# Kernel optimization log

Hardware: AMD Instinct MI355X
Metric: run time of the kernel (lower is better)

## Reference

```python
import jax, jax.numpy as jnp
import numpy as np
from jax import lax

WS = 4
HEADS = 8
DIM = 256
EPS = 1e-5


def _rel_index(ws):
    coords = np.stack(np.meshgrid(np.arange(ws), np.arange(ws), indexing='ij')).reshape(2, -1)
    rc = (coords[:, :, None] - coords[:, None, :]).transpose(1, 2, 0).astype(np.int64)
    rc[..., 0] += ws - 1
    rc[..., 1] += ws - 1
    rc[..., 0] *= 2 * ws - 1
    return jnp.asarray(rc.sum(-1))  # (ws*ws, ws*ws)

REL_IDX = _rel_index(WS)


def _bn(x, g, b, m, v):
    # inference BatchNorm2d, eps=1e-5
    s = g / jnp.sqrt(v + EPS)
    return x * s[None, :, None, None] + (b - m * s)[None, :, None, None]


def setup_inputs() -> dict:
    key = jax.random.key(0)
    ks = jax.random.split(key, 8)
    C = DIM
    return {
        'x': jax.random.normal(ks[0], (4, C, 256, 256), jnp.float32),
        'qkv_w': jax.random.normal(ks[1], (3 * C, C), jnp.float32) * 0.05,
        'qkv_b': jax.random.normal(ks[2], (3 * C,), jnp.float32) * 0.02,
        'rel_bias_table': jax.random.normal(ks[3], ((2 * WS - 1) ** 2, HEADS), jnp.float32) * 0.02,
        'gaze_pw': jax.random.normal(ks[4], (C, C), jnp.float32) * 0.05,
        'gaze_dw': jax.random.normal(ks[5], (C, 1, 3, 3), jnp.float32) * 0.05,
        'gaze_bn_g': jnp.ones((C,), jnp.float32),
        'gaze_bn_b': jnp.zeros((C,), jnp.float32),
        'gaze_bn_m': jnp.zeros((C,), jnp.float32),
        'gaze_bn_v': jnp.ones((C,), jnp.float32),
        'proj_w': jax.random.normal(ks[6], (C, C), jnp.float32) * 0.05,
        'proj_bn_g': jnp.ones((C,), jnp.float32),
        'proj_bn_b': jnp.zeros((C,), jnp.float32),
        'proj_bn_m': jnp.zeros((C,), jnp.float32),
        'proj_bn_v': jnp.ones((C,), jnp.float32),
    }


def reference(x, qkv_w, qkv_b, rel_bias_table, gaze_pw, gaze_dw, gaze_bn_g, gaze_bn_b, gaze_bn_m, gaze_bn_v, proj_w, proj_bn_g, proj_bn_b, proj_bn_m, proj_bn_v):
    B, C, H, W = x.shape
    ws, h = WS, HEADS
    d = C // h
    hh, ww = H // ws, W // ws  # H,W divisible by ws -> reflect pad in original is a no-op
    scale = d ** -0.5

    # qkv 1x1 conv
    qkv = jnp.einsum('bchw,oc->bohw', x, qkv_w) + qkv_b[None, :, None, None]
    # 'b (qkv h d) (hh ws1) (ww ws2) -> qkv (b hh ww) h (ws1 ws2) d'
    qkv = qkv.reshape(B, 3, h, d, hh, ws, ww, ws)
    qkv = qkv.transpose(1, 0, 4, 6, 2, 5, 7, 3).reshape(3, B * hh * ww, h, ws * ws, d)
    q, k, v = qkv[0], qkv[1], qkv[2]

    dots = jnp.einsum('nhqd,nhkd->nhqk', q, k) * scale
    bias = rel_bias_table[REL_IDX.reshape(-1)].reshape(ws * ws, ws * ws, h).transpose(2, 0, 1)
    attn = jax.nn.softmax(dots + bias[None], axis=-1)
    o = jnp.einsum('nhqk,nhkd->nhqd', attn, v)

    def win2img(t):  # '(b hh ww) h (ws1 ws2) d -> b (h d) (hh ws1) (ww ws2)'
        return t.reshape(B, hh, ww, h, ws, ws, d).transpose(0, 3, 6, 1, 4, 2, 5).reshape(B, C, H, W)

    attn_img = win2img(o)
    v_img = win2img(v)

    # gaze = SeparableConvBN: 1x1 pointwise -> 3x3 depthwise -> BN
    vg = jnp.einsum('bchw,oc->bohw', v_img, gaze_pw)
    vg = lax.conv_general_dilated(vg, gaze_dw, (1, 1), ((1, 1), (1, 1)),
                                  feature_group_count=C,
                                  dimension_numbers=('NCHW', 'OIHW', 'NCHW'))
    v_gaze = v_img + _bn(vg, gaze_bn_g, gaze_bn_b, gaze_bn_m, gaze_bn_v)

    # attn_x: reflect-pad bottom 1, AvgPool2d((ws,1), stride 1, pad (ws//2-1,0)), count_include_pad
    ax = jnp.pad(attn_img, ((0, 0), (0, 0), (0, 1), (0, 0)), mode='reflect')
    ax = lax.reduce_window(ax, 0.0, lax.add, (1, 1, ws, 1), (1, 1, 1, 1),
                           ((0, 0), (0, 0), (ws // 2 - 1, ws // 2 - 1), (0, 0))) / ws
    ay = jnp.pad(attn_img, ((0, 0), (0, 0), (0, 0), (0, 1)), mode='reflect')
    ay = lax.reduce_window(ay, 0.0, lax.add, (1, 1, 1, ws), (1, 1, 1, 1),
                           ((0, 0), (0, 0), (0, 0), (ws // 2 - 1, ws // 2 - 1))) / ws

    out = ax + ay + v_gaze
    out = jnp.pad(out, ((0, 0), (0, 0), (0, 1), (0, 1)), mode='reflect')  # pad_out
    out = jnp.einsum('bchw,oc->bohw', out, proj_w)  # proj 1x1 conv (no bias)
    out = _bn(out, proj_bn_g, proj_bn_b, proj_bn_m, proj_bn_v)
    # proj_drop is identity in eval mode
    return out[:, :, :H, :W]
```

## Files before the change

kernel.cpp:

```cpp
#include <hip/hip_runtime.h>


typedef float  f32x4  __attribute__((ext_vector_type(4)));
typedef __bf16 bf16x8 __attribute__((ext_vector_type(8)));
typedef __bf16 bf16x4 __attribute__((ext_vector_type(4)));

#define HW 65536
#define EPSF 1e-5f

__global__ __launch_bounds__(256) void k_prep(
    const float* __restrict__ qkv_w, const float* __restrict__ qkv_b,
    const float* __restrict__ rel_tab,
    const float* __restrict__ gaze_pw, const float* __restrict__ gaze_dw,
    const float* __restrict__ g_g, const float* __restrict__ g_b,
    const float* __restrict__ g_m, const float* __restrict__ g_v,
    const float* __restrict__ proj_w,
    const float* __restrict__ p_g, const float* __restrict__ p_b,
    const float* __restrict__ p_m, const float* __restrict__ p_v,
    __bf16* Wqkv, __bf16* Wpw, __bf16* Wproj,
    float* bqkv, float* biasT, float* dwf, float* bias_g, float* bias_p)
{
  int i = blockIdx.x * 256 + threadIdx.x;
  if (i < 196608) { Wqkv[i] = (__bf16)qkv_w[i]; return; }
  i -= 196608;
  if (i < 65536) { Wpw[i] = (__bf16)gaze_pw[i]; return; }
  i -= 65536;
  if (i < 65536) {
    int o = i >> 8;
    float s = p_g[o] * rsqrtf(p_v[o] + EPSF);
    Wproj[i] = (__bf16)(proj_w[i] * s);
    return;
  }
  i -= 65536;
  if (i < 768) { bqkv[i] = qkv_b[i]; return; }
  i -= 768;
  if (i < 2048) {
    int h = i >> 8, q = (i >> 4) & 15, k = i & 15;
    int rel = ((q >> 2) - (k >> 2) + 3) * 7 + ((q & 3) - (k & 3) + 3);
    biasT[i] = rel_tab[rel * 8 + h];
    return;
  }
  i -= 2048;
  if (i < 2304) {
    int c = i / 9;
    float s = g_g[c] * rsqrtf(g_v[c] + EPSF);
    dwf[i] = gaze_dw[i] * s;
    return;
  }
  i -= 2304;
  if (i < 256) {
    float s = g_g[i] * rsqrtf(g_v[i] + EPSF);
    bias_g[i] = g_b[i] - g_m[i] * s;
    return;
  }
  i -= 256;
  if (i < 256) {
    float s = p_g[i] * rsqrtf(p_v[i] + EPSF);
    bias_p[i] = p_b[i] - p_m[i] * s;
    return;
  }
}

#define K2_SMEM 145408

__global__ __launch_bounds__(512, 2) void k_qkv_attn(
    const float* __restrict__ x, const __bf16* __restrict__ Wqkv,
    const float* __restrict__ bqkv, const float* __restrict__ biasT,
    __bf16* __restrict__ attn_img, __bf16* __restrict__ v_img)
{
  extern __shared__ char smem[];
  __bf16* Xs  = (__bf16*)smem;
  __bf16* QKs = Xs + 64 * 264;
  __bf16* Vs  = QKs + 64 * 520;
  __bf16* Ps  = Vs + 256 * 72;
  __bf16* Os  = QKs;

  const int tid  = threadIdx.x;
  const int lane = tid & 63, wid = tid >> 6;
  const int mrow = lane & 15, kgrp = lane >> 4;
  const int b = blockIdx.z, h0 = blockIdx.y * 4, w0 = blockIdx.x * 16;

  {
    bf16x4 z4;
    z4[0] = z4[1] = z4[2] = z4[3] = (__bf16)0.f;
    *(bf16x4*)(Vs + (tid >> 1) * 72 + 64 + (tid & 1) * 4) = z4;
    bf16x8 z8;
#pragma unroll
    for (int j = 0; j < 8; ++j) z8[j] = (__bf16)0.f;
    *(bf16x8*)(Ps + tid * 8) = z8;
  }

  const float* xb = x + (size_t)b * 256 * HW + (size_t)h0 * 256 + w0;
#pragma unroll
  for (int it = 0; it < 8; ++it) {
    int idx = tid + it * 512;
    int c = idx >> 4, r = (idx >> 2) & 3, g = idx & 3;
    f32x4 v = *(const f32x4*)(xb + (size_t)c * HW + r * 256 + g * 4);
    int p = r * 16 + g * 4;
    Xs[(p + 0) * 264 + c] = (__bf16)v[0];
    Xs[(p + 1) * 264 + c] = (__bf16)v[1];
    Xs[(p + 2) * 264 + c] = (__bf16)v[2];
    Xs[(p + 3) * 264 + c] = (__bf16)v[3];
  }
  __syncthreads();

  for (int co = 0; co < 6; ++co) {
    f32x4 acc[4] = {{0.f,0.f,0.f,0.f},{0.f,0.f,0.f,0.f},
                    {0.f,0.f,0.f,0.f},{0.f,0.f,0.f,0.f}};
    const int ob = co * 128 + wid * 16;
    const __bf16* wp = Wqkv + (size_t)(ob + mrow) * 256 + kgrp * 8;
#pragma unroll
    for (int ks = 0; ks < 8; ++ks) {
      bf16x8 af = *(const bf16x8*)(wp + ks * 32);
#pragma unroll
      for (int j = 0; j < 4; ++j) {
        bf16x8 bm = *(const bf16x8*)(Xs + (j * 16 + mrow) * 264 + ks * 32 + kgrp * 8);
        acc[j] = __builtin_amdgcn_mfma_f32_16x16x32_bf16(af, bm, acc[j], 0, 0, 0);
      }
    }
    f32x4 bi = *(const f32x4*)(bqkv + ob + kgrp * 4);
    if (co < 4) {
      float sc = (co < 2) ? 0.17677669529663687f : 1.0f;
#pragma unroll
      for (int j = 0; j < 4; ++j) {
        int p = j * 16 + mrow;
        bf16x4 pk;
#pragma unroll
        for (int t = 0; t < 4; ++t) pk[t] = (__bf16)((acc[j][t] + bi[t]) * sc);
        *(bf16x4*)(QKs + p * 520 + ob + kgrp * 4) = pk;
      }
    } else {
      int cb = ob - 512 + kgrp * 4;
#pragma unroll
      for (int j = 0; j < 4; ++j) {
        int p = j * 16 + mrow;
#pragma unroll
        for (int t = 0; t < 4; ++t)
          Vs[(cb + t) * 72 + p] = (__bf16)(acc[j][t] + bi[t]);
      }
    }
  }
  __syncthreads();

  bf16x4 osav[4][2];
#pragma unroll
  for (int u = 0; u < 4; ++u) {
    int wh = wid * 4 + u;
    int win = wh >> 3, head = wh & 7;
    int ptok = (mrow >> 2) * 16 + win * 4 + (mrow & 3);
    bf16x8 kf = *(const bf16x8*)(QKs + ptok * 520 + 256 + head * 32 + kgrp * 8);
    bf16x8 qf = *(const bf16x8*)(QKs + ptok * 520 + head * 32 + kgrp * 8);
    f32x4 z4 = {0.f, 0.f, 0.f, 0.f};
    f32x4 d = __builtin_amdgcn_mfma_f32_16x16x32_bf16(kf, qf, z4, 0, 0, 0);
    f32x4 bt = *(const f32x4*)(biasT + head * 256 + mrow * 16 + kgrp * 4);
    float s0 = d[0] + bt[0], s1 = d[1] + bt[1], s2 = d[2] + bt[2], s3 = d[3] + bt[3];
    float mx = fmaxf(fmaxf(s0, s1), fmaxf(s2, s3));
    mx = fmaxf(mx, __shfl_xor(mx, 16));
    mx = fmaxf(mx, __shfl_xor(mx, 32));
    float e0 = __expf(s0 - mx), e1 = __expf(s1 - mx);
    float e2 = __expf(s2 - mx), e3 = __expf(s3 - mx);
    float sm = e0 + e1 + e2 + e3;
    sm += __shfl_xor(sm, 16);
    sm += __shfl_xor(sm, 32);
    float inv = 1.0f / sm;
    bf16x4 pk;
    pk[0] = (__bf16)(e0 * inv); pk[1] = (__bf16)(e1 * inv);
    pk[2] = (__bf16)(e2 * inv); pk[3] = (__bf16)(e3 * inv);
    *(bf16x4*)(Ps + wid * 512 + mrow * 32 + kgrp * 4) = pk;
    bf16x8 pf = *(const bf16x8*)(Ps + wid * 512 + mrow * 32 + kgrp * 8);
#pragma unroll
    for (int dt = 0; dt < 2; ++dt) {
      int c = head * 32 + dt * 16 + mrow;
      bf16x4 va = *(const bf16x4*)(Vs + c * 72 + kgrp * 32 + win * 4);
      bf16x4 vb = *(const bf16x4*)(Vs + c * 72 + kgrp * 32 + 16 + win * 4);
      bf16x8 vf;
#pragma unroll
      for (int t = 0; t < 4; ++t) { vf[t] = va[t]; vf[4 + t] = vb[t]; }
      f32x4 o = __builtin_amdgcn_mfma_f32_16x16x32_bf16(pf, vf, z4, 0, 0, 0);
      bf16x4 ok;
#pragma unroll
      for (int t = 0; t < 4; ++t) ok[t] = (__bf16)o[t];
      osav[u][dt] = ok;
    }
  }
  __syncthreads();
#pragma unroll
  for (int u = 0; u < 4; ++u) {
    int wh = wid * 4 + u, win = wh >> 3, head = wh & 7;
#pragma unroll
    for (int dt = 0; dt < 2; ++dt) {
      int c = head * 32 + dt * 16 + mrow;
      *(bf16x4*)(Os + c * 72 + kgrp * 16 + win * 4) = osav[u][dt];
    }
  }
  __syncthreads();

#pragma unroll
  for (int it = 0; it < 4; ++it) {
    int idx = tid + it * 512;
    int c = idx >> 3, seg = idx & 7;
    bf16x8 o8 = *(const bf16x8*)(Os + c * 72 + seg * 8);
    bf16x8 v8 = *(const bf16x8*)(Vs + c * 72 + seg * 8);
    size_t g = ((size_t)(b * 256 + c) * 256 + h0 + (seg >> 1)) * 256 + w0 + (seg & 1) * 8;
    *(bf16x8*)(attn_img + g) = o8;
    *(bf16x8*)(v_img + g) = v8;
  }
}

__global__ __launch_bounds__(256, 4) void k_pw(
    const __bf16* __restrict__ vimg, const __bf16* __restrict__ Wpw,
    __bf16* __restrict__ vg)
{
  __shared__ __bf16 Xs[64 * 264];
  const int tid = threadIdx.x, lane = tid & 63, wid = tid >> 6;
  const int mrow = lane & 15, kgrp = lane >> 4;
  const int b = blockIdx.z, h = blockIdx.y, w0 = blockIdx.x * 64;
  const size_t rowbase = ((size_t)(b * 256) * 256 + h) * 256 + w0;
#pragma unroll
  for (int it = 0; it < 8; ++it) {
    int idx = tid + it * 256;
    int c = idx >> 3, g = idx & 7;
    bf16x8 v = *(const bf16x8*)(vimg + rowbase + (size_t)c * HW + g * 8);
#pragma unroll
    for (int j = 0; j < 8; ++j) Xs[(g * 8 + j) * 264 + c] = v[j];
  }
  __syncthreads();
  for (int oh = 0; oh < 2; ++oh) {
    int o0 = oh * 128 + wid * 32;
    f32x4 acc[2][4];
#pragma unroll
    for (int mt = 0; mt < 2; ++mt)
#pragma unroll
      for (int nt = 0; nt < 4; ++nt) acc[mt][nt] = (f32x4){0.f, 0.f, 0.f, 0.f};
#pragma unroll
    for (int ks = 0; ks < 8; ++ks) {
      bf16x8 af[2], bm[4];
#pragma unroll
      for (int mt = 0; mt < 2; ++mt)
        af[mt] = *(const bf16x8*)(Wpw + (size_t)(o0 + mt * 16 + mrow) * 256 + ks * 32 + kgrp * 8);
#pragma unroll
      for (int nt = 0; nt < 4; ++nt)
        bm[nt] = *(const bf16x8*)(Xs + (nt * 16 + mrow) * 264 + ks * 32 + kgrp * 8);
#pragma unroll
      for (int mt = 0; mt < 2; ++mt)
#pragma unroll
        for (int nt = 0; nt < 4; ++nt)
          acc[mt][nt] = __builtin_amdgcn_mfma_f32_16x16x32_bf16(af[mt], bm[nt], acc[mt][nt], 0, 0, 0);
    }
#pragma unroll
    for (int mt = 0; mt < 2; ++mt)
#pragma unroll
      for (int nt = 0; nt < 4; ++nt)
#pragma unroll
        for (int t = 0; t < 4; ++t) {
          int o = o0 + mt * 16 + kgrp * 4 + t;
          int p = nt * 16 + mrow;
          vg[rowbase + (size_t)o * HW + p] = (__bf16)acc[mt][nt][t];
        }
  }
}

__global__ __launch_bounds__(256, 4) void k_mix(
    const __bf16* __restrict__ vg, const __bf16* __restrict__ attn,
    const __bf16* __restrict__ vimg, const float* __restrict__ dwf,
    const float* __restrict__ bias_g, __bf16* __restrict__ tout)
{
  __shared__ __bf16 VgS[18 * 256];
  __shared__ __bf16 AtS[19 * 256];
  __shared__ __bf16 ViS[16 * 256];
  const int tid = threadIdx.x;
  const int b = blockIdx.z, c = blockIdx.y, h0 = blockIdx.x * 16;
  const size_t plane = (size_t)(b * 256 + c) * HW;

  for (int idx = tid; idx < 576; idx += 256) {
    int row = idx >> 5, g = idx & 31;
    int hg = h0 - 1 + row;
    bf16x8 v;
#pragma unroll
    for (int j = 0; j < 8; ++j) v[j] = (__bf16)0.f;
    if (hg >= 0 && hg < 256)
      v = *(const bf16x8*)(vg + plane + (size_t)hg * 256 + g * 8);
    *(bf16x8*)(VgS + row * 256 + g * 8) = v;
  }
  for (int idx = tid; idx < 608; idx += 256) {
    int row = idx >> 5, g = idx & 31;
    int hg = h0 - 1 + row;
    bf16x8 v;
#pragma unroll
    for (int j = 0; j < 8; ++j) v[j] = (__bf16)0.f;
    if (hg >= 0 && hg <= 256) {
      int hs = (hg == 256) ? 254 : hg;
      v = *(const bf16x8*)(attn + plane + (size_t)hs * 256 + g * 8);
    }
    *(bf16x8*)(AtS + row * 256 + g * 8) = v;
  }
  for (int idx = tid; idx < 512; idx += 256) {
    int row = idx >> 5, g = idx & 31;
    *(bf16x8*)(ViS + row * 256 + g * 8) =
        *(const bf16x8*)(vimg + plane + (size_t)(h0 + row) * 256 + g * 8);
  }
  float kw[9];
#pragma unroll
  for (int i = 0; i < 9; ++i) kw[i] = dwf[c * 9 + i];
  const float bg = bias_g[c];
  __syncthreads();

  const int hl = tid >> 4, wb = (tid & 15) * 16;
  const __bf16* v0 = VgS + hl * 256;
  const __bf16* v1 = v0 + 256;
  const __bf16* v2 = v1 + 256;
  const __bf16* a0 = AtS + hl * 256;
  const __bf16* a1 = a0 + 256;
  const __bf16* a2 = a1 + 256;
  const __bf16* a3 = a2 + 256;
  const __bf16* vi = ViS + hl * 256;
  const size_t orow = plane + (size_t)(h0 + hl) * 256;
  for (int w8 = 0; w8 < 2; ++w8) {
    bf16x8 res;
#pragma unroll
    for (int j = 0; j < 8; ++j) {
      int w = wb + w8 * 8 + j;
      int xm = w - 1, xp = w + 1;
      float conv = kw[1] * (float)v0[w] + kw[4] * (float)v1[w] + kw[7] * (float)v2[w];
      if (xm >= 0)
        conv += kw[0] * (float)v0[xm] + kw[3] * (float)v1[xm] + kw[6] * (float)v2[xm];
      if (xp < 256)
        conv += kw[2] * (float)v0[xp] + kw[5] * (float)v1[xp] + kw[8] * (float)v2[xp];
      float ax = 0.25f * ((float)a0[w] + (float)a1[w] + (float)a2[w] + (float)a3[w]);
      float aym = (w >= 1) ? (float)a1[w - 1] : 0.f;
      float ay1 = (w + 1 <= 255) ? (float)a1[w + 1] : (float)a1[254];
      float ay2;
      int x2 = w + 2;
      if (x2 <= 255) ay2 = (float)a1[x2];
      else if (x2 == 256) ay2 = (float)a1[254];
      else ay2 = 0.f;
      float ay = 0.25f * (aym + (float)a1[w] + ay1 + ay2);
      res[j] = (__bf16)((float)vi[w] + conv + bg + ax + ay);
    }
    *(bf16x8*)(tout + orow + wb + w8 * 8) = res;
  }
}

__global__ __launch_bounds__(256, 4) void k_proj(
    const __bf16* __restrict__ tin, const __bf16* __restrict__ Wp,
    const float* __restrict__ bias_p, float* __restrict__ out)
{
  __shared__ __bf16 Xs[64 * 264];
  const int tid = threadIdx.x, lane = tid & 63, wid = tid >> 6;
  const int mrow = lane & 15, kgrp = lane >> 4;
  const int b = blockIdx.z, h = blockIdx.y, w0 = blockIdx.x * 64;
  const size_t rowbase = ((size_t)(b * 256) * 256 + h) * 256 + w0;
#pragma unroll
  for (int it = 0; it < 8; ++it) {
    int idx = tid + it * 256;
    int c = idx >> 3, g = idx & 7;
    bf16x8 v = *(const bf16x8*)(tin + rowbase + (size_t)c * HW + g * 8);
#pragma unroll
    for (int j = 0; j < 8; ++j) Xs[(g * 8 + j) * 264 + c] = v[j];
  }
  __syncthreads();
  for (int oh = 0; oh < 2; ++oh) {
    int o0 = oh * 128 + wid * 32;
    f32x4 acc[2][4];
#pragma unroll
    for (int mt = 0; mt < 2; ++mt)
#pragma unroll
      for (int nt = 0; nt < 4; ++nt) acc[mt][nt] = (f32x4){0.f, 0.f, 0.f, 0.f};
#pragma unroll
    for (int ks = 0; ks < 8; ++ks) {
      bf16x8 af[2], bm[4];
#pragma unroll
      for (int mt = 0; mt < 2; ++mt)
        af[mt] = *(const bf16x8*)(Wp + (size_t)(o0 + mt * 16 + mrow) * 256 + ks * 32 + kgrp * 8);
#pragma unroll
      for (int nt = 0; nt < 4; ++nt)
        bm[nt] = *(const bf16x8*)(Xs + (nt * 16 + mrow) * 264 + ks * 32 + kgrp * 8);
#pragma unroll
      for (int mt = 0; mt < 2; ++mt)
#pragma unroll
        for (int nt = 0; nt < 4; ++nt)
          acc[mt][nt] = __builtin_amdgcn_mfma_f32_16x16x32_bf16(af[mt], bm[nt], acc[mt][nt], 0, 0, 0);
    }
#pragma unroll
    for (int mt = 0; mt < 2; ++mt) {
      f32x4 bi = *(const f32x4*)(bias_p + o0 + mt * 16 + kgrp * 4);
#pragma unroll
      for (int nt = 0; nt < 4; ++nt)
#pragma unroll
        for (int t = 0; t < 4; ++t) {
          int o = o0 + mt * 16 + kgrp * 4 + t;
          int p = nt * 16 + mrow;
          out[rowbase + (size_t)o * HW + p] = acc[mt][nt][t] + bi[t];
        }
    }
  }
}

extern "C" void kernel_launch(void* const* d_in, const int* in_sizes, int n_in,
                              void* d_out, int out_size, void* d_ws, size_t ws_size,
                              hipStream_t stream) {
  const float* x      = (const float*)d_in[0];
  const float* qkv_w  = (const float*)d_in[1];
  const float* qkv_b  = (const float*)d_in[2];
  const float* rel    = (const float*)d_in[3];
  const float* gpw    = (const float*)d_in[4];
  const float* gdw    = (const float*)d_in[5];
  const float* gg     = (const float*)d_in[6];
  const float* gb     = (const float*)d_in[7];
  const float* gm     = (const float*)d_in[8];
  const float* gv     = (const float*)d_in[9];
  const float* pw     = (const float*)d_in[10];
  const float* pg     = (const float*)d_in[11];
  const float* pb     = (const float*)d_in[12];
  const float* pm     = (const float*)d_in[13];
  const float* pv     = (const float*)d_in[14];

  char* ws = (char*)d_ws;
  __bf16* Wqkv   = (__bf16*)(ws + 0);
  __bf16* Wpw    = (__bf16*)(ws + 393216);
  __bf16* Wproj  = (__bf16*)(ws + 524288);
  float*  bqkv   = (float*)(ws + 655360);
  float*  biasT  = (float*)(ws + 658432);
  float*  dwf    = (float*)(ws + 666624);
  float*  bias_g = (float*)(ws + 675840);
  float*  bias_p = (float*)(ws + 676864);
  __bf16* attn_img = (__bf16*)(ws + (1 << 20));
  __bf16* v_img    = attn_img + 67108864;
  __bf16* vg       = v_img + 67108864;
  __bf16* tbuf     = vg + 67108864;
  float* out = (float*)d_out;

  (void)hipFuncSetAttribute((const void*)k_qkv_attn,
                            hipFuncAttributeMaxDynamicSharedMemorySize, K2_SMEM);

  k_prep<<<1302, 256, 0, stream>>>(qkv_w, qkv_b, rel, gpw, gdw, gg, gb, gm, gv,
                                   pw, pg, pb, pm, pv,
                                   Wqkv, Wpw, Wproj, bqkv, biasT, dwf, bias_g, bias_p);

  dim3 g2(16, 64, 4);
  k_qkv_attn<<<g2, 512, K2_SMEM, stream>>>(x, Wqkv, bqkv, biasT, attn_img, v_img);

  dim3 g3(4, 256, 4);
  k_pw<<<g3, 256, 0, stream>>>(v_img, Wpw, vg);

  dim3 g4(16, 256, 4);
  k_mix<<<g4, 256, 0, stream>>>(vg, attn_img, v_img, dwf, bias_g, tbuf);

  k_proj<<<g3, 256, 0, stream>>>(tbuf, Wproj, bias_p, out);
}
```

Measured before the change: 1.754 ms.

## Stage pointwise and proj GEMM inputs through LDS transpose with vectorized stores

The pw and proj kernels now load input channels in two 128-channel chunks into a natural-layout LDS buffer, then transpose it into a pixel-major buffer using 16-byte writes, replacing scattered 2-byte LDS stores. The MFMA operands are swapped so each lane's accumulator holds consecutive pixels, which lets the epilogue write bf16x4 or f32x4 vectors instead of scalar strided stores. The qkv kernel's x load is also changed to scalar per-column loads. This costs extra syncs and an additional LDS pass, and the scalar x loads in the qkv kernel may reduce global load width.

```diff
diff --git a/kernel.cpp b/kernel.cpp
--- a/kernel.cpp
+++ b/kernel.cpp
@@ -93,14 +93,12 @@
   const float* xb = x + (size_t)b * 256 * HW + (size_t)h0 * 256 + w0;
 #pragma unroll
   for (int it = 0; it < 8; ++it) {
-    int idx = tid + it * 512;
-    int c = idx >> 4, r = (idx >> 2) & 3, g = idx & 3;
-    f32x4 v = *(const f32x4*)(xb + (size_t)c * HW + r * 256 + g * 4);
-    int p = r * 16 + g * 4;
-    Xs[(p + 0) * 264 + c] = (__bf16)v[0];
-    Xs[(p + 1) * 264 + c] = (__bf16)v[1];
-    Xs[(p + 2) * 264 + c] = (__bf16)v[2];
-    Xs[(p + 3) * 264 + c] = (__bf16)v[3];
+    int idx = it * 512 + tid;
+    int c = idx >> 4, col = idx & 15;
+    const float* px = xb + (size_t)c * HW + col;
+#pragma unroll
+    for (int r = 0; r < 4; ++r)
+      Xs[(r * 16 + col) * 264 + c] = (__bf16)px[(size_t)r * 256];
   }
   __syncthreads();
 
@@ -211,52 +209,75 @@
     const __bf16* __restrict__ vimg, const __bf16* __restrict__ Wpw,
     __bf16* __restrict__ vg)
 {
-  __shared__ __bf16 Xs[64 * 264];
+  __shared__ __bf16 Ns[128 * 72];
+  __shared__ __bf16 Xs[64 * 136];
   const int tid = threadIdx.x, lane = tid & 63, wid = tid >> 6;
   const int mrow = lane & 15, kgrp = lane >> 4;
   const int b = blockIdx.z, h = blockIdx.y, w0 = blockIdx.x * 64;
   const size_t rowbase = ((size_t)(b * 256) * 256 + h) * 256 + w0;
-#pragma unroll
-  for (int it = 0; it < 8; ++it) {
-    int idx = tid + it * 256;
-    int c = idx >> 3, g = idx & 7;
-    bf16x8 v = *(const bf16x8*)(vimg + rowbase + (size_t)c * HW + g * 8);
-#pragma unroll
-    for (int j = 0; j < 8; ++j) Xs[(g * 8 + j) * 264 + c] = v[j];
-  }
-  __syncthreads();
+
+  f32x4 acc[2][2][4];
+#pragma unroll
+  for (int oh = 0; oh < 2; ++oh)
+#pragma unroll
+    for (int mt = 0; mt < 2; ++mt)
+#pragma unroll
+      for (int nt = 0; nt < 4; ++nt) acc[oh][mt][nt] = (f32x4){0.f, 0.f, 0.f, 0.f};
+
+  for (int kc = 0; kc < 2; ++kc) {
+#pragma unroll
+    for (int it = 0; it < 4; ++it) {
+      int idx = it * 256 + tid;
+      int cl = idx >> 3, g = idx & 7;
+      bf16x8 v = *(const bf16x8*)(vimg + rowbase + (size_t)(kc * 128 + cl) * HW + g * 8);
+      *(bf16x8*)(Ns + cl * 72 + g * 8) = v;
+    }
+    __syncthreads();
+#pragma unroll
+    for (int it = 0; it < 4; ++it) {
+      int task = it * 256 + tid;
+      int px = task & 63, oct = task >> 6;
+      int c0 = oct * 8;
+      bf16x8 r;
+#pragma unroll
+      for (int j = 0; j < 8; ++j) r[j] = Ns[(c0 + j) * 72 + px];
+      *(bf16x8*)(Xs + px * 136 + c0) = r;
+    }
+    __syncthreads();
+#pragma unroll
+    for (int oh = 0; oh < 2; ++oh) {
+      const int o0 = oh * 128 + wid * 32;
+#pragma unroll
+      for (int ks = 0; ks < 4; ++ks) {
+        bf16x8 af[2], bm[4];
+#pragma unroll
+        for (int mt = 0; mt < 2; ++mt)
+          af[mt] = *(const bf16x8*)(Wpw + (size_t)(o0 + mt * 16 + mrow) * 256 + kc * 128 + ks * 32 + kgrp * 8);
+#pragma unroll
+        for (int nt = 0; nt < 4; ++nt)
+          bm[nt] = *(const bf16x8*)(Xs + (nt * 16 + mrow) * 136 + ks * 32 + kgrp * 8);
+#pragma unroll
+        for (int mt = 0; mt < 2; ++mt)
+#pragma unroll
+          for (int nt = 0; nt < 4; ++nt)
+            acc[oh][mt][nt] = __builtin_amdgcn_mfma_f32_16x16x32_bf16(bm[nt], af[mt], acc[oh][mt][nt], 0, 0, 0);
+      }
+    }
+    __syncthreads();
+  }
+#pragma unroll
   for (int oh = 0; oh < 2; ++oh) {
-    int o0 = oh * 128 + wid * 32;
-    f32x4 acc[2][4];
-#pragma unroll
-    for (int mt = 0; mt < 2; ++mt)
-#pragma unroll
-      for (int nt = 0; nt < 4; ++nt) acc[mt][nt] = (f32x4){0.f, 0.f, 0.f, 0.f};
-#pragma unroll
-    for (int ks = 0; ks < 8; ++ks) {
-      bf16x8 af[2], bm[4];
-#pragma unroll
-      for (int mt = 0; mt < 2; ++mt)
-        af[mt] = *(const bf16x8*)(Wpw + (size_t)(o0 + mt * 16 + mrow) * 256 + ks * 32 + kgrp * 8);
-#pragma unroll
-      for (int nt = 0; nt < 4; ++nt)
-        bm[nt] = *(const bf16x8*)(Xs + (nt * 16 + mrow) * 264 + ks * 32 + kgrp * 8);
-#pragma unroll
-      for (int mt = 0; mt < 2; ++mt)
-#pragma unroll
-        for (int nt = 0; nt < 4; ++nt)
-          acc[mt][nt] = __builtin_amdgcn_mfma_f32_16x16x32_bf16(af[mt], bm[nt], acc[mt][nt], 0, 0, 0);
-    }
-#pragma unroll
-    for (int mt = 0; mt < 2; ++mt)
-#pragma unroll
-      for (int nt = 0; nt < 4; ++nt)
-#pragma unroll
-        for (int t = 0; t < 4; ++t) {
-          int o = o0 + mt * 16 + kgrp * 4 + t;
-          int p = nt * 16 + mrow;
-          vg[rowbase + (size_t)o * HW + p] = (__bf16)acc[mt][nt][t];
-        }
+#pragma unroll
+    for (int mt = 0; mt < 2; ++mt) {
+      int o = oh * 128 + wid * 32 + mt * 16 + mrow;
+#pragma unroll
+      for (int nt = 0; nt < 4; ++nt) {
+        bf16x4 pk;
+#pragma unroll
+        for (int t = 0; t < 4; ++t) pk[t] = (__bf16)acc[oh][mt][nt][t];
+        *(bf16x4*)(vg + rowbase + (size_t)o * HW + nt * 16 + kgrp * 4) = pk;
+      }
+    }
   }
 }
 
@@ -345,53 +366,75 @@
     const __bf16* __restrict__ tin, const __bf16* __restrict__ Wp,
     const float* __restrict__ bias_p, float* __restrict__ out)
 {
-  __shared__ __bf16 Xs[64 * 264];
+  __shared__ __bf16 Ns[128 * 72];
+  __shared__ __bf16 Xs[64 * 136];
   const int tid = threadIdx.x, lane = tid & 63, wid = tid >> 6;
   const int mrow = lane & 15, kgrp = lane >> 4;
   const int b = blockIdx.z, h = blockIdx.y, w0 = blockIdx.x * 64;
   const size_t rowbase = ((size_t)(b * 256) * 256 + h) * 256 + w0;
-#pragma unroll
-  for (int it = 0; it < 8; ++it) {
-    int idx = tid + it * 256;
-    int c = idx >> 3, g = idx & 7;
-    bf16x8 v = *(const bf16x8*)(tin + rowbase + (size_t)c * HW + g * 8);
-#pragma unroll
-    for (int j = 0; j < 8; ++j) Xs[(g * 8 + j) * 264 + c] = v[j];
-  }
-  __syncthreads();
+
+  f32x4 acc[2][2][4];
+#pragma unroll
+  for (int oh = 0; oh < 2; ++oh)
+#pragma unroll
+    for (int mt = 0; mt < 2; ++mt)
+#pragma unroll
+      for (int nt = 0; nt < 4; ++nt) acc[oh][mt][nt] = (f32x4){0.f, 0.f, 0.f, 0.f};
+
+  for (int kc = 0; kc < 2; ++kc) {
+#pragma unroll
+    for (int it = 0; it < 4; ++it) {
+      int idx = it * 256 + tid;
+      int cl = idx >> 3, g = idx & 7;
+      bf16x8 v = *(const bf16x8*)(tin + rowbase + (size_t)(kc * 128 + cl) * HW + g * 8);
+      *(bf16x8*)(Ns + cl * 72 + g * 8) = v;
+    }
+    __syncthreads();
+#pragma unroll
+    for (int it = 0; it < 4; ++it) {
+      int task = it * 256 + tid;
+      int px = task & 63, oct = task >> 6;
+      int c0 = oct * 8;
+      bf16x8 r;
+#pragma unroll
+      for (int j = 0; j < 8; ++j) r[j] = Ns[(c0 + j) * 72 + px];
+      *(bf16x8*)(Xs + px * 136 + c0) = r;
+    }
+    __syncthreads();
+#pragma unroll
+    for (int oh = 0; oh < 2; ++oh) {
+      const int o0 = oh * 128 + wid * 32;
+#pragma unroll
+      for (int ks = 0; ks < 4; ++ks) {
+        bf16x8 af[2], bm[4];
+#pragma unroll
+        for (int mt = 0; mt < 2; ++mt)
+          af[mt] = *(const bf16x8*)(Wp + (size_t)(o0 + mt * 16 + mrow) * 256 + kc * 128 + ks * 32 + kgrp * 8);
+#pragma unroll
+        for (int nt = 0; nt < 4; ++nt)
+          bm[nt] = *(const bf16x8*)(Xs + (nt * 16 + mrow) * 136 + ks * 32 + kgrp * 8);
+#pragma unroll
+        for (int mt = 0; mt < 2; ++mt)
+#pragma unroll
+          for (int nt = 0; nt < 4; ++nt)
+            acc[oh][mt][nt] = __builtin_amdgcn_mfma_f32_16x16x32_bf16(bm[nt], af[mt], acc[oh][mt][nt], 0, 0, 0);
+      }
+    }
+    __syncthreads();
+  }
+#pragma unroll
   for (int oh = 0; oh < 2; ++oh) {
-    int o0 = oh * 128 + wid * 32;
-    f32x4 acc[2][4];
-#pragma unroll
-    for (int mt = 0; mt < 2; ++mt)
-#pragma unroll
-      for (int nt = 0; nt < 4; ++nt) acc[mt][nt] = (f32x4){0.f, 0.f, 0.f, 0.f};
-#pragma unroll
-    for (int ks = 0; ks < 8; ++ks) {
-      bf16x8 af[2], bm[4];
-#pragma unroll
-      for (int mt = 0; mt < 2; ++mt)
-        af[mt] = *(const bf16x8*)(Wp + (size_t)(o0 + mt * 16 + mrow) * 256 + ks * 32 + kgrp * 8);
-#pragma unroll
-      for (int nt = 0; nt < 4; ++nt)
-        bm[nt] = *(const bf16x8*)(Xs + (nt * 16 + mrow) * 264 + ks * 32 + kgrp * 8);
-#pragma unroll
-      for (int mt = 0; mt < 2; ++mt)
-#pragma unroll
-        for (int nt = 0; nt < 4; ++nt)
-          acc[mt][nt] = __builtin_amdgcn_mfma_f32_16x16x32_bf16(af[mt], bm[nt], acc[mt][nt], 0, 0, 0);
-    }
 #pragma unroll
     for (int mt = 0; mt < 2; ++mt) {
-      f32x4 bi = *(const f32x4*)(bias_p + o0 + mt * 16 + kgrp * 4);
-#pragma unroll
-      for (int nt = 0; nt < 4; ++nt)
-#pragma unroll
-        for (int t = 0; t < 4; ++t) {
-          int o = o0 + mt * 16 + kgrp * 4 + t;
-          int p = nt * 16 + mrow;
-          out[rowbase + (size_t)o * HW + p] = acc[mt][nt][t] + bi[t];
-        }
+      int o = oh * 128 + wid * 32 + mt * 16 + mrow;
+      float bb = bias_p[o];
+#pragma unroll
+      for (int nt = 0; nt < 4; ++nt) {
+        f32x4 r;
+#pragma unroll
+        for (int t = 0; t < 4; ++t) r[t] = acc[oh][mt][nt][t] + bb;
+        *(f32x4*)(out + rowbase + (size_t)o * HW + nt * 16 + kgrp * 4) = r;
+      }
     }
   }
 }
```

Result: faster. 1.463 ms (-16.6%).
